# Optimization experiments

Measured on AMD Instinct MI355X. Metric: run time of the kernel, lower is better.

## Reference

```python
import jax, jax.numpy as jnp
import numpy as np

B, S, D, H = 2, 2048, 1024, 16
HEAD_DIM = D // H
MAX_REL = 64  # max_relative_position in source


def setup_inputs() -> dict:
    key = jax.random.key(0)
    ks = jax.random.split(key, 8)
    std = 0.02
    return {
        "query": jax.random.normal(ks[0], (B, S, D), jnp.float32),
        "key": jax.random.normal(ks[1], (B, S, D), jnp.float32),
        "value": jax.random.normal(ks[2], (B, S, D), jnp.float32),
        "attention_mask": jnp.zeros((B, 1, 1, S), jnp.float32),
        "Wq": jax.random.normal(ks[3], (D, D), jnp.float32) * std,
        "bq": jnp.zeros((D,), jnp.float32),
        "Wk": jax.random.normal(ks[4], (D, D), jnp.float32) * std,
        "bk": jnp.zeros((D,), jnp.float32),
        "Wv": jax.random.normal(ks[5], (D, D), jnp.float32) * std,
        "bv": jnp.zeros((D,), jnp.float32),
        "rel_table": jax.random.normal(ks[6], (2 * MAX_REL + 1, HEAD_DIM), jnp.float32) * std,
    }


def _split_heads(x, b):
    # [B,S,D] -> [B,H,S,d]
    return x.reshape(b, -1, H, HEAD_DIM).transpose(0, 2, 1, 3)


def reference(query, key, value, attention_mask, Wq, bq, Wk, bk, Wv, bv, rel_table):
    b, s, _ = query.shape
    q = _split_heads(query @ Wq + bq, b)   # [B,H,S,d]
    k = _split_heads(key @ Wk + bk, b)
    v = _split_heads(value @ Wv + bv, b)

    scores = jnp.einsum("bhqd,bhkd->bhqk", q, k)  # [B,H,S,S]

    # relative-position key bias: rel_k[q_idx, k_idx] = table[clip(k-q)+MAX_REL]
    idx = jnp.arange(s)
    dist = jnp.clip(idx[None, :] - idx[:, None], -MAX_REL, MAX_REL) + MAX_REL  # [S,S]
    rel_k = rel_table[dist]  # [S,S,d]
    scores = scores + jnp.einsum("bhqd,qkd->bhqk", q, rel_k)

    scores = scores / jnp.sqrt(jnp.asarray(HEAD_DIM, scores.dtype))
    scores = scores + attention_mask  # additive mask, broadcast [B,1,1,S]

    probs = jax.nn.softmax(scores, axis=-1)  # dropout is identity (p=0 / eval)
    ctx = jnp.einsum("bhqk,bhkd->bhqd", probs, v)
    ctx = ctx.transpose(0, 2, 1, 3).reshape(b, s, H * HEAD_DIM)
    return ctx
```

## Files before the change

kernel.cpp:

```cpp
#include <hip/hip_runtime.h>
#include <hip/hip_bf16.h>

#define BB 2
#define SS 2048
#define DD 1024
#define HH 16
#define HD 64
#define NREL 129
#define QRS 132
#define LOG2E 1.4426950408889634f
#define SCALEQ (LOG2E / 8.0f)
#define KVB 131072l

typedef short s8v __attribute__((ext_vector_type(8)));
typedef short s4v __attribute__((ext_vector_type(4)));
typedef float f4 __attribute__((ext_vector_type(4)));

#define MFMA_BF16 __builtin_amdgcn_mfma_f32_16x16x32_bf16

__device__ __forceinline__ float bf2f(unsigned short u) {
  union { unsigned int i; float f; } x; x.i = ((unsigned int)u) << 16; return x.f;
}
__device__ __forceinline__ unsigned short f2bf(float f) {
  union { float f; unsigned int i; } x; x.f = f;
  unsigned int r = x.i + 0x7fffu + ((x.i >> 16) & 1u);
  return (unsigned short)(r >> 16);
}
__device__ __forceinline__ unsigned int pk2bf(float a, float b) {
  union { __hip_bfloat162 h2; unsigned int u; } c;
  c.h2 = __float22bfloat162_rn(float2{a, b});
  return c.u;
}
__device__ __forceinline__ void gl_lds16(const void* g, void* l) {
  __builtin_amdgcn_global_load_lds(
      (const __attribute__((address_space(1))) unsigned int*)g,
      (__attribute__((address_space(3))) unsigned int*)l, 16, 0, 0);
}

__global__ __launch_bounds__(256) void cvt_x(
    const float* __restrict__ xq, const float* __restrict__ xk,
    const float* __restrict__ xv, const float* __restrict__ mask,
    unsigned short* __restrict__ xb, float* __restrict__ mkg) {
  const int z = blockIdx.y;
  const float* in = (z == 0) ? xq : (z == 1) ? xk : xv;
  unsigned short* out = xb + (long)z * 4096 * DD;
  const long i = ((long)blockIdx.x * 256 + threadIdx.x) * 8;
  f4 a = *(const f4*)(in + i);
  f4 b = *(const f4*)(in + i + 4);
  unsigned int u[4];
  u[0] = pk2bf(a[0], a[1]); u[1] = pk2bf(a[2], a[3]);
  u[2] = pk2bf(b[0], b[1]); u[3] = pk2bf(b[2], b[3]);
  *(s8v*)(out + i) = *(s8v*)u;
  if (z == 0 && blockIdx.x < BB) {
    const int row = blockIdx.x;
    const long j = (long)row * SS + threadIdx.x * 8;
    f4 ma = *(const f4*)(mask + j);
    f4 mb = *(const f4*)(mask + j + 4);
    #pragma unroll
    for (int e = 0; e < 4; ++e) {
      mkg[j + e] = ma[e] * LOG2E;
      mkg[j + 4 + e] = mb[e] * LOG2E;
    }
  }
}

__global__ __launch_bounds__(256) void cvt_w(
    const float* __restrict__ Wq, const float* __restrict__ Wk,
    const float* __restrict__ Wv, unsigned short* __restrict__ WTt) {
  __shared__ unsigned short tile[64][72];
  const int z = blockIdx.z;
  const float* in = (z == 0) ? Wq : (z == 1) ? Wk : Wv;
  unsigned short* out = WTt + (long)z * 1048576;
  const int c0 = blockIdx.x * 64, r0 = blockIdx.y * 64;
  const int t = threadIdx.x;
  const int r = t >> 2;
  #pragma unroll
  for (int j = 0; j < 4; ++j) {
    int cc = (t & 3) * 16 + j * 4;
    f4 v = *(const f4*)(in + (long)(r0 + r) * DD + c0 + cc);
    #pragma unroll
    for (int e = 0; e < 4; ++e) tile[r][cc + e] = f2bf(v[e]);
  }
  __syncthreads();
  const int c = t >> 2;
  #pragma unroll
  for (int h = 0; h < 2; ++h) {
    int r8 = (t & 3) + 4 * h;
    unsigned short vals[8];
    #pragma unroll
    for (int j = 0; j < 8; ++j) vals[j] = tile[r8 * 8 + j][c];
    int n = c0 + c, kb = r0 + r8 * 8;
    long off = ((long)(n >> 7) * 131072) + ((kb >> 6) * 8192) +
               (((kb & 63) >> 3) * 1024) + ((n & 127) * 8);
    *(s8v*)(out + off) = *(s8v*)vals;
  }
}

__global__ __launch_bounds__(256, 4) void proj_gemm(
    const unsigned short* __restrict__ Xb, const unsigned short* __restrict__ WTt,
    const float* __restrict__ bq, const float* __restrict__ bk,
    const float* __restrict__ bv,
    unsigned short* __restrict__ qbuf, unsigned short* __restrict__ ktile,
    unsigned short* __restrict__ vtile) {
  __shared__ __align__(16) unsigned short wt[8][128][8];
  unsigned short* wtf = &wt[0][0][0];
  const int z = blockIdx.z;
  const unsigned short* X = Xb + (long)z * 4096 * DD;
  const unsigned short* WTz = WTt + (long)z * 1048576;
  const float* bias = (z == 0) ? bq : (z == 1) ? bk : bv;

  const int n0 = blockIdx.x * 128, m0 = blockIdx.y * 128;
  const int t = threadIdx.x, w = t >> 6, l = t & 63;
  const int lm = l & 15, qd = l >> 4;

  f4 acc[8][2];
  #pragma unroll
  for (int i = 0; i < 8; ++i) { acc[i][0] = (f4)0.0f; acc[i][1] = (f4)0.0f; }

  const unsigned short* x0 = X + (long)(m0 + w * 32 + lm) * DD;
  const unsigned short* x1 = x0 + 16 * DD;
  const unsigned short* wtile0 = WTz + (long)(n0 >> 7) * 131072;

  for (int k0 = 0; k0 < DD; k0 += 64) {
    __syncthreads();
    const unsigned short* tb = wtile0 + (k0 >> 6) * 8192;
    #pragma unroll
    for (int i = 0; i < 4; ++i) {
      int idx = w * 4 + i;
      gl_lds16(tb + idx * 512 + l * 8, wtf + idx * 512);
    }
    s8v a00 = *(const s8v*)(x0 + k0 + qd * 8);
    s8v a01 = *(const s8v*)(x0 + k0 + 32 + qd * 8);
    s8v a10 = *(const s8v*)(x1 + k0 + qd * 8);
    s8v a11 = *(const s8v*)(x1 + k0 + 32 + qd * 8);
    asm volatile("s_waitcnt vmcnt(0)" ::: "memory");
    __syncthreads();
    #pragma unroll
    for (int cb = 0; cb < 8; ++cb) {
      s8v b0 = *(const s8v*)&wt[qd][cb * 16 + lm][0];
      s8v b1 = *(const s8v*)&wt[4 + qd][cb * 16 + lm][0];
      acc[cb][0] = MFMA_BF16(a00, b0, acc[cb][0], 0, 0, 0);
      acc[cb][0] = MFMA_BF16(a01, b1, acc[cb][0], 0, 0, 0);
      acc[cb][1] = MFMA_BF16(a10, b0, acc[cb][1], 0, 0, 0);
      acc[cb][1] = MFMA_BF16(a11, b1, acc[cb][1], 0, 0, 0);
    }
  }
  if (z == 0) {
    #pragma unroll
    for (int cb = 0; cb < 8; ++cb) {
      int n = n0 + cb * 16 + lm;
      float bvv = bias[n];
      int hh = n >> 6, d = n & 63;
      #pragma unroll
      for (int ms = 0; ms < 2; ++ms) {
        #pragma unroll
        for (int r = 0; r < 4; ++r) {
          int m = m0 + w * 32 + ms * 16 + qd * 4 + r;
          int bidx = m >> 11, s = m & (SS - 1);
          qbuf[((long)(bidx * HH + hh) * SS + s) * HD + d] =
              f2bf((acc[cb][ms][r] + bvv) * SCALEQ);
        }
      }
    }
  } else if (z == 1) {
    #pragma unroll
    for (int cb = 0; cb < 8; ++cb) {
      int n = n0 + cb * 16 + lm;
      float bvv = bias[n];
      int hh = n >> 6, d = n & 63;
      int c = d >> 3, e = d & 7;
      #pragma unroll
      for (int ms = 0; ms < 2; ++ms) {
        #pragma unroll
        for (int r = 0; r < 4; ++r) {
          int m = m0 + w * 32 + ms * 16 + qd * 4 + r;
          int bidx = m >> 11, s = m & (SS - 1);
          long bh = bidx * HH + hh;
          ktile[bh * KVB + (s >> 6) * 4096 + c * 512 + (s & 63) * 8 + e] =
              f2bf(acc[cb][ms][r] + bvv);
        }
      }
    }
  } else {
    #pragma unroll
    for (int cb = 0; cb < 8; ++cb) {
      int n = n0 + cb * 16 + lm;
      float bvv = bias[n];
      int hh = n >> 6, d = n & 63;
      #pragma unroll
      for (int ms = 0; ms < 2; ++ms) {
        int m = m0 + w * 32 + ms * 16 + qd * 4;
        int bidx = m >> 11, s = m & (SS - 1);
        long bh = bidx * HH + hh;
        unsigned short o4[4];
        #pragma unroll
        for (int r = 0; r < 4; ++r) o4[r] = f2bf(acc[cb][ms][r] + bvv);
        *(s4v*)&vtile[bh * KVB + (s >> 6) * 4096 + ((s & 63) >> 3) * 512 +
                      d * 8 + (s & 7)] = *(s4v*)o4;
      }
    }
  }
}

__global__ __launch_bounds__(256, 2) void attn(
    const unsigned short* __restrict__ qb, const unsigned short* __restrict__ ktile,
    const unsigned short* __restrict__ vtile, const float* __restrict__ tableF,
    const float* __restrict__ mkg, unsigned short* __restrict__ qrg,
    float* __restrict__ out) {
  __shared__ __align__(16) unsigned short ks[2][8][64][8];
  __shared__ __align__(16) unsigned short vs[2][8][64][8];
  __shared__ __align__(16) unsigned short pbuf[4][16][40];

  const int bh = blockIdx.y, b = bh >> 4, h = bh & 15;
  const int q0 = blockIdx.x * 128;
  const int t = threadIdx.x, w = t >> 6, l = t & 63;
  const int lm = l & 15, qd = l >> 4;
  const int qw = q0 + w * 32;
  const int qc0 = w * 32 + lm, qc1 = qc0 + 16;

  const unsigned short* kkb = ktile + (long)bh * KVB;
  const unsigned short* vvb = vtile + (long)bh * KVB;
  unsigned short* qblk = qrg + ((long)(bh * 16 + blockIdx.x)) * 128 * QRS;

  #pragma unroll
  for (int i = 0; i < 2; ++i) {
    int c = 2 * w + i;
    gl_lds16(kkb + c * 512 + l * 8, &ks[0][c][0][0]);
    gl_lds16(vvb + c * 512 + l * 8, &vs[0][c][0][0]);
  }

  const unsigned short* qrow = qb + ((long)bh * SS + qw + lm) * HD;
  const s8v qa0 = *(const s8v*)(qrow + qd * 8);
  const s8v qa1 = *(const s8v*)(qrow + 32 + qd * 8);
  const s8v qb0 = *(const s8v*)(qrow + 16 * HD + qd * 8);
  const s8v qb1 = *(const s8v*)(qrow + 16 * HD + 32 + qd * 8);

  #pragma unroll
  for (int cb = 0; cb < 9; ++cb) {
    int dist = cb * 16 + lm;
    int dc = dist > NREL - 1 ? NREL - 1 : dist;
    const float* trow = tableF + dc * HD;
    f4 t0 = *(const f4*)(trow + qd * 8);
    f4 t1 = *(const f4*)(trow + qd * 8 + 4);
    f4 t2 = *(const f4*)(trow + 32 + qd * 8);
    f4 t3 = *(const f4*)(trow + 32 + qd * 8 + 4);
    unsigned int tb[8];
    tb[0] = pk2bf(t0[0], t0[1]); tb[1] = pk2bf(t0[2], t0[3]);
    tb[2] = pk2bf(t1[0], t1[1]); tb[3] = pk2bf(t1[2], t1[3]);
    tb[4] = pk2bf(t2[0], t2[1]); tb[5] = pk2bf(t2[2], t2[3]);
    tb[6] = pk2bf(t3[0], t3[1]); tb[7] = pk2bf(t3[2], t3[3]);
    s8v b0 = *(s8v*)tb, b1 = *(s8v*)(tb + 4);
    f4 c0 = MFMA_BF16(qa0, b0, (f4)0.0f, 0, 0, 0);
    c0 = MFMA_BF16(qa1, b1, c0, 0, 0, 0);
    f4 c1 = MFMA_BF16(qb0, b0, (f4)0.0f, 0, 0, 0);
    c1 = MFMA_BF16(qb1, b1, c1, 0, 0, 0);
    if (dist <= NREL - 1) {
      #pragma unroll
      for (int r = 0; r < 4; ++r) {
        qblk[(w * 32 + qd * 4 + r) * QRS + dist] = f2bf(c0[r]);
        qblk[(w * 32 + 16 + qd * 4 + r) * QRS + dist] = f2bf(c1[r]);
      }
    }
  }
  asm volatile("s_waitcnt vmcnt(0)" ::: "memory");
  __syncthreads();

  const unsigned short* qr0 = qblk + qc0 * QRS;
  const unsigned short* qr1 = qblk + qc1 * QRS;
  const float bLo0 = bf2f(qr0[0]), bHi0 = bf2f(qr0[128]);
  const float bLo1 = bf2f(qr1[0]), bHi1 = bf2f(qr1[128]);
  const float* mrow = mkg + b * SS;

  float m0_ = -1e30f, l0_ = 0.0f, m1_ = -1e30f, l1_ = 0.0f;
  f4 c40[4], c41[4];
  #pragma unroll
  for (int i = 0; i < 4; ++i) { c40[i] = (f4)0.0f; c41[i] = (f4)0.0f; }

  for (int rr = 0; rr < 32; ++rr) {
    const int kk = rr << 6;
    const int buf = rr & 1;
    if (rr < 31) {
      const int nb = buf ^ 1;
      const unsigned short* kg = kkb + (rr + 1) * 4096;
      const unsigned short* vg = vvb + (rr + 1) * 4096;
      #pragma unroll
      for (int i = 0; i < 2; ++i) {
        int c = 2 * w + i;
        gl_lds16(kg + c * 512 + l * 8, &ks[nb][c][0][0]);
        gl_lds16(vg + c * 512 + l * 8, &vs[nb][c][0][0]);
      }
    }
    f4 st0[4], st1[4];
    #pragma unroll
    for (int tt = 0; tt < 4; ++tt) {
      s8v k0v = *(const s8v*)&ks[buf][qd][tt * 16 + lm][0];
      s8v k1v = *(const s8v*)&ks[buf][4 + qd][tt * 16 + lm][0];
      st0[tt] = MFMA_BF16(k0v, qa0, (f4)0.0f, 0, 0, 0);
      st0[tt] = MFMA_BF16(k1v, qa1, st0[tt], 0, 0, 0);
      st1[tt] = MFMA_BF16(k0v, qb0, (f4)0.0f, 0, 0, 0);
      st1[tt] = MFMA_BF16(k1v, qb1, st1[tt], 0, 0, 0);
    }
    float z0[16], z1[16];
    const int kw = kk - qw;
    if (kw >= 96) {
      #pragma unroll
      for (int tt = 0; tt < 4; ++tt) {
        f4 mv = *(const f4*)&mrow[kk + tt * 16 + qd * 4];
        #pragma unroll
        for (int r = 0; r < 4; ++r) {
          z0[tt * 4 + r] = st0[tt][r] + bHi0 + mv[r];
          z1[tt * 4 + r] = st1[tt][r] + bHi1 + mv[r];
        }
      }
    } else if (kw <= -128) {
      #pragma unroll
      for (int tt = 0; tt < 4; ++tt) {
        f4 mv = *(const f4*)&mrow[kk + tt * 16 + qd * 4];
        #pragma unroll
        for (int r = 0; r < 4; ++r) {
          z0[tt * 4 + r] = st0[tt][r] + bLo0 + mv[r];
          z1[tt * 4 + r] = st1[tt][r] + bLo1 + mv[r];
        }
      }
    } else {
      const int db0 = kw - lm + 64 + qd * 4;
      #pragma unroll
      for (int tt = 0; tt < 4; ++tt) {
        f4 mv = *(const f4*)&mrow[kk + tt * 16 + qd * 4];
        #pragma unroll
        for (int r = 0; r < 4; ++r) {
          int du = db0 + tt * 16 + r;
          int d0 = du < 0 ? 0 : (du > 128 ? 128 : du);
          int d1 = du - 16; d1 = d1 < 0 ? 0 : (d1 > 128 ? 128 : d1);
          z0[tt * 4 + r] = st0[tt][r] + bf2f(qr0[d0]) + mv[r];
          z1[tt * 4 + r] = st1[tt][r] + bf2f(qr1[d1]) + mv[r];
        }
      }
    }
    float tm0 = z0[0], tm1 = z1[0];
    #pragma unroll
    for (int i = 1; i < 16; ++i) {
      tm0 = fmaxf(tm0, z0[i]);
      tm1 = fmaxf(tm1, z1[i]);
    }
    tm0 = fmaxf(tm0, __shfl_xor(tm0, 16));
    tm0 = fmaxf(tm0, __shfl_xor(tm0, 32));
    tm1 = fmaxf(tm1, __shfl_xor(tm1, 16));
    tm1 = fmaxf(tm1, __shfl_xor(tm1, 32));
    float mn0 = fmaxf(m0_, tm0), mn1 = fmaxf(m1_, tm1);
    float al0 = __builtin_amdgcn_exp2f(m0_ - mn0);
    float al1 = __builtin_amdgcn_exp2f(m1_ - mn1);
    m0_ = mn0; m1_ = mn1;
    float s0 = 0.0f, s1 = 0.0f;
    #pragma unroll
    for (int i = 0; i < 16; ++i) {
      z0[i] = __builtin_amdgcn_exp2f(z0[i] - mn0); s0 += z0[i];
      z1[i] = __builtin_amdgcn_exp2f(z1[i] - mn1); s1 += z1[i];
    }
    s0 += __shfl_xor(s0, 16);
    s0 += __shfl_xor(s0, 32);
    s1 += __shfl_xor(s1, 16);
    s1 += __shfl_xor(s1, 32);
    l0_ = l0_ * al0 + s0; l1_ = l1_ * al1 + s1;
    #pragma unroll
    for (int db = 0; db < 4; ++db)
      #pragma unroll
      for (int r = 0; r < 4; ++r) { c40[db][r] *= al0; c41[db][r] *= al1; }

    {
      s8v va[4];
      #pragma unroll
      for (int db = 0; db < 4; ++db)
        va[db] = *(const s8v*)&vs[buf][qd][db * 16 + lm][0];
      *(unsigned int*)&pbuf[w][lm][qd * 4] = pk2bf(z0[0], z0[1]);
      *(unsigned int*)&pbuf[w][lm][qd * 4 + 2] = pk2bf(z0[2], z0[3]);
      *(unsigned int*)&pbuf[w][lm][16 + qd * 4] = pk2bf(z0[4], z0[5]);
      *(unsigned int*)&pbuf[w][lm][16 + qd * 4 + 2] = pk2bf(z0[6], z0[7]);
      asm volatile("s_waitcnt lgkmcnt(0)" ::: "memory");
      {
        s8v pa = *(const s8v*)&pbuf[w][lm][qd * 8];
        #pragma unroll
        for (int db = 0; db < 4; ++db)
          c40[db] = MFMA_BF16(va[db], pa, c40[db], 0, 0, 0);
      }
      *(unsigned int*)&pbuf[w][lm][qd * 4] = pk2bf(z1[0], z1[1]);
      *(unsigned int*)&pbuf[w][lm][qd * 4 + 2] = pk2bf(z1[2], z1[3]);
      *(unsigned int*)&pbuf[w][lm][16 + qd * 4] = pk2bf(z1[4], z1[5]);
      *(unsigned int*)&pbuf[w][lm][16 + qd * 4 + 2] = pk2bf(z1[6], z1[7]);
      asm volatile("s_waitcnt lgkmcnt(0)" ::: "memory");
      {
        s8v pa = *(const s8v*)&pbuf[w][lm][qd * 8];
        #pragma unroll
        for (int db = 0; db < 4; ++db)
          c41[db] = MFMA_BF16(va[db], pa, c41[db], 0, 0, 0);
      }
    }
    {
      s8v vb[4];
      #pragma unroll
      for (int db = 0; db < 4; ++db)
        vb[db] = *(const s8v*)&vs[buf][4 + qd][db * 16 + lm][0];
      *(unsigned int*)&pbuf[w][lm][qd * 4] = pk2bf(z0[8], z0[9]);
      *(unsigned int*)&pbuf[w][lm][qd * 4 + 2] = pk2bf(z0[10], z0[11]);
      *(unsigned int*)&pbuf[w][lm][16 + qd * 4] = pk2bf(z0[12], z0[13]);
      *(unsigned int*)&pbuf[w][lm][16 + qd * 4 + 2] = pk2bf(z0[14], z0[15]);
      asm volatile("s_waitcnt lgkmcnt(0)" ::: "memory");
      {
        s8v pb = *(const s8v*)&pbuf[w][lm][qd * 8];
        #pragma unroll
        for (int db = 0; db < 4; ++db)
          c40[db] = MFMA_BF16(vb[db], pb, c40[db], 0, 0, 0);
      }
      *(unsigned int*)&pbuf[w][lm][qd * 4] = pk2bf(z1[8], z1[9]);
      *(unsigned int*)&pbuf[w][lm][qd * 4 + 2] = pk2bf(z1[10], z1[11]);
      *(unsigned int*)&pbuf[w][lm][16 + qd * 4] = pk2bf(z1[12], z1[13]);
      *(unsigned int*)&pbuf[w][lm][16 + qd * 4 + 2] = pk2bf(z1[14], z1[15]);
      asm volatile("s_waitcnt lgkmcnt(0)" ::: "memory");
      {
        s8v pb = *(const s8v*)&pbuf[w][lm][qd * 8];
        #pragma unroll
        for (int db = 0; db < 4; ++db)
          c41[db] = MFMA_BF16(vb[db], pb, c41[db], 0, 0, 0);
      }
    }
    asm volatile("s_waitcnt vmcnt(0)" ::: "memory");
    __syncthreads();
  }

  const float inv0 = 1.0f / l0_, inv1 = 1.0f / l1_;
  float* ob0 = out + ((long)b * SS + q0 + qc0) * DD + h * HD;
  float* ob1 = out + ((long)b * SS + q0 + qc1) * DD + h * HD;
  #pragma unroll
  for (int db = 0; db < 4; ++db) {
    f4 o0, o1;
    #pragma unroll
    for (int r = 0; r < 4; ++r) {
      o0[r] = c40[db][r] * inv0;
      o1[r] = c41[db][r] * inv1;
    }
    *(f4*)(ob0 + db * 16 + qd * 4) = o0;
    *(f4*)(ob1 + db * 16 + qd * 4) = o1;
  }
}

extern "C" void kernel_launch(void* const* d_in, const int* in_sizes, int n_in,
                              void* d_out, int out_size, void* d_ws, size_t ws_size,
                              hipStream_t stream) {
  const float* query = (const float*)d_in[0];
  const float* key   = (const float*)d_in[1];
  const float* value = (const float*)d_in[2];
  const float* mask  = (const float*)d_in[3];
  const float* Wq    = (const float*)d_in[4];
  const float* bq    = (const float*)d_in[5];
  const float* Wk    = (const float*)d_in[6];
  const float* bk    = (const float*)d_in[7];
  const float* Wv    = (const float*)d_in[8];
  const float* bv    = (const float*)d_in[9];
  const float* table = (const float*)d_in[10];

  char* ws = (char*)d_ws;
  unsigned short* WTt   = (unsigned short*)(ws);
  float*          mkg   = (float*)(ws + (7l << 20));
  unsigned short* Xb    = (unsigned short*)(ws + (8l << 20));
  unsigned short* qrg   = (unsigned short*)(ws + (8l << 20));
  unsigned short* qbuf  = (unsigned short*)(ws + (32l << 20));
  unsigned short* ktile = (unsigned short*)(ws + (40l << 20));
  unsigned short* vtile = (unsigned short*)(ws + (48l << 20));

  cvt_x<<<dim3(2048, 3, 1), 256, 0, stream>>>(query, key, value, mask, Xb, mkg);

  cvt_w<<<dim3(16, 16, 3), 256, 0, stream>>>(Wq, Wk, Wv, WTt);

  proj_gemm<<<dim3(8, 32, 3), 256, 0, stream>>>(Xb, WTt, bq, bk, bv,
                                                qbuf, ktile, vtile);

  attn<<<dim3(16, 32, 1), 256, 0, stream>>>(qbuf, ktile, vtile, table,
                                            mkg, qrg, (float*)d_out);
}
```

Before: 245.5 us.

## Keep relative bias in LDS, lazy softmax rescale, merge P staging

Stores the per-block query-relative-table products in shared memory instead of a global scratch buffer, removing global stores and reloads in the diagonal band. Adds a lazy online-softmax rescale that only updates the running max when it grows by more than a threshold, skipping the accumulator rescale most iterations. Writes both row groups' probabilities to separate LDS buffers so one wait covers both MFMA batches. Increases LDS use per block, which could pressure occupancy.

```diff
diff --git a/kernel.cpp b/kernel.cpp
--- a/kernel.cpp
+++ b/kernel.cpp
@@ -7,7 +7,6 @@
 #define HH 16
 #define HD 64
 #define NREL 129
-#define QRS 132
 #define LOG2E 1.4426950408889634f
 #define SCALEQ (LOG2E / 8.0f)
 #define KVB 131072l
@@ -205,11 +204,12 @@
 __global__ __launch_bounds__(256, 2) void attn(
     const unsigned short* __restrict__ qb, const unsigned short* __restrict__ ktile,
     const unsigned short* __restrict__ vtile, const float* __restrict__ tableF,
-    const float* __restrict__ mkg, unsigned short* __restrict__ qrg,
-    float* __restrict__ out) {
+    const float* __restrict__ mkg, float* __restrict__ out) {
   __shared__ __align__(16) unsigned short ks[2][8][64][8];
   __shared__ __align__(16) unsigned short vs[2][8][64][8];
-  __shared__ __align__(16) unsigned short pbuf[4][16][40];
+  __shared__ __align__(16) unsigned short qr2[NREL][130];
+  __shared__ __align__(16) unsigned short pb0[4][16][40];
+  __shared__ __align__(16) unsigned short pb1[4][16][40];
 
   const int bh = blockIdx.y, b = bh >> 4, h = bh & 15;
   const int q0 = blockIdx.x * 128;
@@ -220,7 +220,6 @@
 
   const unsigned short* kkb = ktile + (long)bh * KVB;
   const unsigned short* vvb = vtile + (long)bh * KVB;
-  unsigned short* qblk = qrg + ((long)(bh * 16 + blockIdx.x)) * 128 * QRS;
 
   #pragma unroll
   for (int i = 0; i < 2; ++i) {
@@ -257,18 +256,16 @@
     if (dist <= NREL - 1) {
       #pragma unroll
       for (int r = 0; r < 4; ++r) {
-        qblk[(w * 32 + qd * 4 + r) * QRS + dist] = f2bf(c0[r]);
-        qblk[(w * 32 + 16 + qd * 4 + r) * QRS + dist] = f2bf(c1[r]);
+        qr2[dist][w * 32 + qd * 4 + r] = f2bf(c0[r]);
+        qr2[dist][w * 32 + 16 + qd * 4 + r] = f2bf(c1[r]);
       }
     }
   }
   asm volatile("s_waitcnt vmcnt(0)" ::: "memory");
   __syncthreads();
 
-  const unsigned short* qr0 = qblk + qc0 * QRS;
-  const unsigned short* qr1 = qblk + qc1 * QRS;
-  const float bLo0 = bf2f(qr0[0]), bHi0 = bf2f(qr0[128]);
-  const float bLo1 = bf2f(qr1[0]), bHi1 = bf2f(qr1[128]);
+  const float bLo0 = bf2f(qr2[0][qc0]), bHi0 = bf2f(qr2[128][qc0]);
+  const float bLo1 = bf2f(qr2[0][qc1]), bHi1 = bf2f(qr2[128][qc1]);
   const float* mrow = mkg + b * SS;
 
   float m0_ = -1e30f, l0_ = 0.0f, m1_ = -1e30f, l1_ = 0.0f;
@@ -332,8 +329,8 @@
           int du = db0 + tt * 16 + r;
           int d0 = du < 0 ? 0 : (du > 128 ? 128 : du);
           int d1 = du - 16; d1 = d1 < 0 ? 0 : (d1 > 128 ? 128 : d1);
-          z0[tt * 4 + r] = st0[tt][r] + bf2f(qr0[d0]) + mv[r];
-          z1[tt * 4 + r] = st1[tt][r] + bf2f(qr1[d1]) + mv[r];
+          z0[tt * 4 + r] = st0[tt][r] + bf2f(qr2[d0][qc0]) + mv[r];
+          z1[tt * 4 + r] = st1[tt][r] + bf2f(qr2[d1][qc1]) + mv[r];
         }
       }
     }
@@ -347,80 +344,72 @@
     tm0 = fmaxf(tm0, __shfl_xor(tm0, 32));
     tm1 = fmaxf(tm1, __shfl_xor(tm1, 16));
     tm1 = fmaxf(tm1, __shfl_xor(tm1, 32));
-    float mn0 = fmaxf(m0_, tm0), mn1 = fmaxf(m1_, tm1);
-    float al0 = __builtin_amdgcn_exp2f(m0_ - mn0);
-    float al1 = __builtin_amdgcn_exp2f(m1_ - mn1);
-    m0_ = mn0; m1_ = mn1;
+    if (!__all(tm0 - m0_ <= 8.0f)) {
+      float mn0 = fmaxf(m0_, tm0);
+      float al0 = __builtin_amdgcn_exp2f(m0_ - mn0);
+      m0_ = mn0; l0_ *= al0;
+      #pragma unroll
+      for (int db = 0; db < 4; ++db)
+        #pragma unroll
+        for (int r = 0; r < 4; ++r) c40[db][r] *= al0;
+    }
+    if (!__all(tm1 - m1_ <= 8.0f)) {
+      float mn1 = fmaxf(m1_, tm1);
+      float al1 = __builtin_amdgcn_exp2f(m1_ - mn1);
+      m1_ = mn1; l1_ *= al1;
+      #pragma unroll
+      for (int db = 0; db < 4; ++db)
+        #pragma unroll
+        for (int r = 0; r < 4; ++r) c41[db][r] *= al1;
+    }
     float s0 = 0.0f, s1 = 0.0f;
     #pragma unroll
     for (int i = 0; i < 16; ++i) {
-      z0[i] = __builtin_amdgcn_exp2f(z0[i] - mn0); s0 += z0[i];
-      z1[i] = __builtin_amdgcn_exp2f(z1[i] - mn1); s1 += z1[i];
+      z0[i] = __builtin_amdgcn_exp2f(z0[i] - m0_); s0 += z0[i];
+      z1[i] = __builtin_amdgcn_exp2f(z1[i] - m1_); s1 += z1[i];
     }
     s0 += __shfl_xor(s0, 16);
     s0 += __shfl_xor(s0, 32);
     s1 += __shfl_xor(s1, 16);
     s1 += __shfl_xor(s1, 32);
-    l0_ = l0_ * al0 + s0; l1_ = l1_ * al1 + s1;
-    #pragma unroll
-    for (int db = 0; db < 4; ++db)
-      #pragma unroll
-      for (int r = 0; r < 4; ++r) { c40[db][r] *= al0; c41[db][r] *= al1; }
+    l0_ += s0; l1_ += s1;
 
     {
-      s8v va[4];
-      #pragma unroll
-      for (int db = 0; db < 4; ++db)
-        va[db] = *(const s8v*)&vs[buf][qd][db * 16 + lm][0];
-      *(unsigned int*)&pbuf[w][lm][qd * 4] = pk2bf(z0[0], z0[1]);
-      *(unsigned int*)&pbuf[w][lm][qd * 4 + 2] = pk2bf(z0[2], z0[3]);
-      *(unsigned int*)&pbuf[w][lm][16 + qd * 4] = pk2bf(z0[4], z0[5]);
-      *(unsigned int*)&pbuf[w][lm][16 + qd * 4 + 2] = pk2bf(z0[6], z0[7]);
+      *(unsigned int*)&pb0[w][lm][qd * 4]          = pk2bf(z0[0], z0[1]);
+      *(unsigned int*)&pb0[w][lm][qd * 4 + 2]      = pk2bf(z0[2], z0[3]);
+      *(unsigned int*)&pb0[w][lm][16 + qd * 4]     = pk2bf(z0[4], z0[5]);
+      *(unsigned int*)&pb0[w][lm][16 + qd * 4 + 2] = pk2bf(z0[6], z0[7]);
+      *(unsigned int*)&pb1[w][lm][qd * 4]          = pk2bf(z1[0], z1[1]);
+      *(unsigned int*)&pb1[w][lm][qd * 4 + 2]      = pk2bf(z1[2], z1[3]);
+      *(unsigned int*)&pb1[w][lm][16 + qd * 4]     = pk2bf(z1[4], z1[5]);
+      *(unsigned int*)&pb1[w][lm][16 + qd * 4 + 2] = pk2bf(z1[6], z1[7]);
       asm volatile("s_waitcnt lgkmcnt(0)" ::: "memory");
-      {
-        s8v pa = *(const s8v*)&pbuf[w][lm][qd * 8];
-        #pragma unroll
-        for (int db = 0; db < 4; ++db)
-          c40[db] = MFMA_BF16(va[db], pa, c40[db], 0, 0, 0);
-      }
-      *(unsigned int*)&pbuf[w][lm][qd * 4] = pk2bf(z1[0], z1[1]);
-      *(unsigned int*)&pbuf[w][lm][qd * 4 + 2] = pk2bf(z1[2], z1[3]);
-      *(unsigned int*)&pbuf[w][lm][16 + qd * 4] = pk2bf(z1[4], z1[5]);
-      *(unsigned int*)&pbuf[w][lm][16 + qd * 4 + 2] = pk2bf(z1[6], z1[7]);
+      s8v pa0 = *(const s8v*)&pb0[w][lm][qd * 8];
+      s8v pa1 = *(const s8v*)&pb1[w][lm][qd * 8];
+      #pragma unroll
+      for (int db = 0; db < 4; ++db) {
+        s8v va = *(const s8v*)&vs[buf][qd][db * 16 + lm][0];
+        c40[db] = MFMA_BF16(va, pa0, c40[db], 0, 0, 0);
+        c41[db] = MFMA_BF16(va, pa1, c41[db], 0, 0, 0);
+      }
+    }
+    {
+      *(unsigned int*)&pb0[w][lm][qd * 4]          = pk2bf(z0[8], z0[9]);
+      *(unsigned int*)&pb0[w][lm][qd * 4 + 2]      = pk2bf(z0[10], z0[11]);
+      *(unsigned int*)&pb0[w][lm][16 + qd * 4]     = pk2bf(z0[12], z0[13]);
+      *(unsigned int*)&pb0[w][lm][16 + qd * 4 + 2] = pk2bf(z0[14], z0[15]);
+      *(unsigned int*)&pb1[w][lm][qd * 4]          = pk2bf(z1[8], z1[9]);
+      *(unsigned int*)&pb1[w][lm][qd * 4 + 2]      = pk2bf(z1[10], z1[11]);
+      *(unsigned int*)&pb1[w][lm][16 + qd * 4]     = pk2bf(z1[12], z1[13]);
+      *(unsigned int*)&pb1[w][lm][16 + qd * 4 + 2] = pk2bf(z1[14], z1[15]);
       asm volatile("s_waitcnt lgkmcnt(0)" ::: "memory");
-      {
-        s8v pa = *(const s8v*)&pbuf[w][lm][qd * 8];
-        #pragma unroll
-        for (int db = 0; db < 4; ++db)
-          c41[db] = MFMA_BF16(va[db], pa, c41[db], 0, 0, 0);
-      }
-    }
-    {
-      s8v vb[4];
-      #pragma unroll
-      for (int db = 0; db < 4; ++db)
-        vb[db] = *(const s8v*)&vs[buf][4 + qd][db * 16 + lm][0];
-      *(unsigned int*)&pbuf[w][lm][qd * 4] = pk2bf(z0[8], z0[9]);
-      *(unsigned int*)&pbuf[w][lm][qd * 4 + 2] = pk2bf(z0[10], z0[11]);
-      *(unsigned int*)&pbuf[w][lm][16 + qd * 4] = pk2bf(z0[12], z0[13]);
-      *(unsigned int*)&pbuf[w][lm][16 + qd * 4 + 2] = pk2bf(z0[14], z0[15]);
-      asm volatile("s_waitcnt lgkmcnt(0)" ::: "memory");
-      {
-        s8v pb = *(const s8v*)&pbuf[w][lm][qd * 8];
-        #pragma unroll
-        for (int db = 0; db < 4; ++db)
-          c40[db] = MFMA_BF16(vb[db], pb, c40[db], 0, 0, 0);
-      }
-      *(unsigned int*)&pbuf[w][lm][qd * 4] = pk2bf(z1[8], z1[9]);
-      *(unsigned int*)&pbuf[w][lm][qd * 4 + 2] = pk2bf(z1[10], z1[11]);
-      *(unsigned int*)&pbuf[w][lm][16 + qd * 4] = pk2bf(z1[12], z1[13]);
-      *(unsigned int*)&pbuf[w][lm][16 + qd * 4 + 2] = pk2bf(z1[14], z1[15]);
-      asm volatile("s_waitcnt lgkmcnt(0)" ::: "memory");
-      {
-        s8v pb = *(const s8v*)&pbuf[w][lm][qd * 8];
-        #pragma unroll
-        for (int db = 0; db < 4; ++db)
-          c41[db] = MFMA_BF16(vb[db], pb, c41[db], 0, 0, 0);
+      s8v pB0 = *(const s8v*)&pb0[w][lm][qd * 8];
+      s8v pB1 = *(const s8v*)&pb1[w][lm][qd * 8];
+      #pragma unroll
+      for (int db = 0; db < 4; ++db) {
+        s8v vb = *(const s8v*)&vs[buf][4 + qd][db * 16 + lm][0];
+        c40[db] = MFMA_BF16(vb, pB0, c40[db], 0, 0, 0);
+        c41[db] = MFMA_BF16(vb, pB1, c41[db], 0, 0, 0);
       }
     }
     asm volatile("s_waitcnt vmcnt(0)" ::: "memory");
@@ -462,7 +451,6 @@
   unsigned short* WTt   = (unsigned short*)(ws);
   float*          mkg   = (float*)(ws + (7l << 20));
   unsigned short* Xb    = (unsigned short*)(ws + (8l << 20));
-  unsigned short* qrg   = (unsigned short*)(ws + (8l << 20));
   unsigned short* qbuf  = (unsigned short*)(ws + (32l << 20));
   unsigned short* ktile = (unsigned short*)(ws + (40l << 20));
   unsigned short* vtile = (unsigned short*)(ws + (48l << 20));
@@ -475,5 +463,5 @@
                                                 qbuf, ktile, vtile);
 
   attn<<<dim3(16, 32, 1), 256, 0, stream>>>(qbuf, ktile, vtile, table,
-                                            mkg, qrg, (float*)d_out);
-}
+                                            mkg, (float*)d_out);
+}
```

Result: faster. 232.9 us (-5.2%).
